# Kernel optimization log

Hardware: AMD Instinct MI355X
Metric: run time of the kernel (lower is better)

Reference implementation:

```python
import jax, jax.numpy as jnp
import numpy as np

B, S, D, H, FF = 2, 4096, 1024, 16, 4096
HD = D // H


def _layernorm(x, g, b, eps=1e-5):
    mu = jnp.mean(x, axis=-1, keepdims=True)
    var = jnp.var(x, axis=-1, keepdims=True)
    return (x - mu) * jax.lax.rsqrt(var + eps) * g + b


def setup_inputs() -> dict:
    key = jax.random.key(0)
    ks = jax.random.split(key, 20)
    sd = 1.0 / np.sqrt(D)
    sf = 1.0 / np.sqrt(FF)
    inp = {
        "x": jax.random.normal(ks[0], (B, S, D), jnp.float32),
        # attention projections, stored as [in, out]
        "wq": jax.random.normal(ks[1], (D, D), jnp.float32) * sd,
        "bq": jnp.zeros((D,), jnp.float32),
        "wk": jax.random.normal(ks[2], (D, D), jnp.float32) * sd,
        "bk": jnp.zeros((D,), jnp.float32),
        "wv": jax.random.normal(ks[3], (D, D), jnp.float32) * sd,
        "bv": jnp.zeros((D,), jnp.float32),
        "wo": jax.random.normal(ks[4], (D, D), jnp.float32) * sd,
        "bo": jnp.zeros((D,), jnp.float32),
        # block norm1 (pre-attention)
        "ln1_g": jnp.ones((D,), jnp.float32),
        "ln1_b": jnp.zeros((D,), jnp.float32),
        # FFN internal norm
        "lnf_g": jnp.ones((D,), jnp.float32),
        "lnf_b": jnp.zeros((D,), jnp.float32),
        # gated FFN
        "w1": jax.random.normal(ks[5], (D, FF), jnp.float32) * sd,
        "b1": jnp.zeros((FF,), jnp.float32),
        "wg": jax.random.normal(ks[6], (D, FF), jnp.float32) * sd,
        "bg": jnp.zeros((FF,), jnp.float32),
        "w2": jax.random.normal(ks[7], (FF, D), jnp.float32) * sf,
        "b2": jnp.zeros((D,), jnp.float32),
    }
    return inp


def reference(x, wq, bq, wk, bk, wv, bv, wo, bo, ln1_g, ln1_b,
              lnf_g, lnf_b, w1, b1, wg, bg, w2, b2):
    # pre-norm attention
    residual = x
    h = _layernorm(x, ln1_g, ln1_b)
    q = (h @ wq + bq).reshape(B, S, H, HD).transpose(0, 2, 1, 3)  # [B,H,S,hd]
    k = (h @ wk + bk).reshape(B, S, H, HD).transpose(0, 2, 1, 3)
    v = (h @ wv + bv).reshape(B, S, H, HD).transpose(0, 2, 1, 3)
    scores = jnp.einsum("bhqd,bhkd->bhqk", q, k) / np.sqrt(HD)
    attn = jax.nn.softmax(scores, axis=-1)  # [B,H,S,S] materialized as in torch src
    ctx = jnp.einsum("bhqk,bhkd->bhqd", attn, v)
    ctx = ctx.transpose(0, 2, 1, 3).reshape(B, S, D)
    attn_out = ctx @ wo + bo
    x = residual + attn_out  # dropout = 0 (eval)

    # gated FFN with internal pre-norm and residual
    res2 = x
    h2 = _layernorm(x, lnf_g, lnf_b)
    gate = jax.nn.sigmoid(h2 @ wg + bg)
    up = jax.nn.gelu(h2 @ w1 + b1, approximate=False)
    out = (up * gate) @ w2 + b2
    return out + res2
```

## Files before the change

kernel.cpp:

```cpp
#include <hip/hip_runtime.h>
#include <hip/hip_bf16.h>

#define BB 2
#define SS 4096
#define DD 1024
#define HH 16
#define HD 64
#define FF 4096
#define MM (BB*SS)

typedef __hip_bfloat16 bf16;
typedef __attribute__((ext_vector_type(8))) __bf16 v8bf;
typedef __attribute__((ext_vector_type(4))) float f32x4;
typedef __attribute__((ext_vector_type(16))) float f32x16;
typedef __attribute__((ext_vector_type(8))) unsigned short u16v8;

__device__ __forceinline__ f32x4 mfma16(v8bf a, v8bf b, f32x4 c) {
  return __builtin_amdgcn_mfma_f32_16x16x32_bf16(a, b, c, 0, 0, 0);
}
__device__ __forceinline__ f32x16 mfma32(v8bf a, v8bf b, f32x16 c) {
  return __builtin_amdgcn_mfma_f32_32x32x16_bf16(a, b, c, 0, 0, 0);
}
__device__ __forceinline__ void gload16(const void* g, void* l) {
  __builtin_amdgcn_global_load_lds((const __attribute__((address_space(1))) void*)g,
                                   (__attribute__((address_space(3))) void*)l, 16, 0, 0);
}
__device__ __forceinline__ unsigned cvtpk_bf16(float lo, float hi) {
  unsigned r;
  asm("v_cvt_pk_bf16_f32 %0, %1, %2" : "=v"(r) : "v"(lo), "v"(hi));
  return r;
}

__global__ void k_tcvt(const float* __restrict__ W, bf16* __restrict__ Wt, int K, int N,
                       int pairsel)
{
  __shared__ float tile[32][33];
  const int n0 = blockIdx.x * 32, k0 = blockIdx.y * 32;
  const int tx = threadIdx.x, ty = threadIdx.y;
#pragma unroll
  for (int i = 0; i < 32; i += 8)
    tile[ty + i][tx] = W[(long)(k0 + ty + i) * N + n0 + tx];
  __syncthreads();
#pragma unroll
  for (int i = 0; i < 32; i += 8) {
    long orow = n0 + ty + i;
    if (pairsel >= 0) orow = ((orow >> 6) << 7) + pairsel * 64 + (orow & 63);
    Wt[orow * K + k0 + tx] = __float2bfloat16(tile[tx][ty + i]);
  }
}

__global__ __launch_bounds__(256)
void k_vtrans(const bf16* __restrict__ V, bf16* __restrict__ Vt)
{
  __shared__ bf16 tile[64][72];
  const int s0 = blockIdx.x * 64;
  const int h  = blockIdx.y;
  const int b  = blockIdx.z;
  const int t  = threadIdx.x;
  const int r = t >> 3, c8 = t & 7;
#pragma unroll
  for (int it = 0; it < 2; ++it) {
    const int sr = it * 32 + r;
    const u16v8 v = *(const u16v8*)(V + (long)(b * SS + s0 + sr) * DD + h * 64 + c8 * 8);
#pragma unroll
    for (int e = 0; e < 8; ++e)
      ((unsigned short*)&tile[sr][0])[c8 * 8 + e] = v[e];
  }
  __syncthreads();
#pragma unroll
  for (int it = 0; it < 2; ++it) {
    const int d = it * 32 + r;
    union { unsigned short s[8]; u16v8 v; } o;
#pragma unroll
    for (int e = 0; e < 8; ++e)
      o.s[e] = ((const unsigned short*)tile)[(c8 * 8 + e) * 72 + d];
    *(u16v8*)(Vt + ((long)(b * HH + h) * HD + d) * (long)SS + s0 + c8 * 8) = o.v;
  }
}

__global__ __launch_bounds__(256)
void k_layernorm(const float* __restrict__ x, const float* __restrict__ g,
                 const float* __restrict__ b, bf16* __restrict__ out)
{
  const int row = blockIdx.x;
  const float4 v = ((const float4*)(x + (long)row * DD))[threadIdx.x];
  float s  = v.x + v.y + v.z + v.w;
  float s2 = v.x*v.x + v.y*v.y + v.z*v.z + v.w*v.w;
#pragma unroll
  for (int off = 1; off < 64; off <<= 1) {
    s  += __shfl_xor(s,  off);
    s2 += __shfl_xor(s2, off);
  }
  __shared__ float red[8];
  if ((threadIdx.x & 63) == 0) {
    red[threadIdx.x >> 6]       = s;
    red[(threadIdx.x >> 6) + 4] = s2;
  }
  __syncthreads();
  s  = red[0] + red[1] + red[2] + red[3];
  s2 = red[4] + red[5] + red[6] + red[7];
  const float mu = s * (1.f / DD);
  const float rs = rsqrtf(s2 * (1.f / DD) - mu * mu + 1e-5f);
  const float4 gv = ((const float4*)g)[threadIdx.x];
  const float4 bv = ((const float4*)b)[threadIdx.x];
  bf16* op = out + (long)row * DD + threadIdx.x * 4;
  op[0] = __float2bfloat16((v.x - mu) * rs * gv.x + bv.x);
  op[1] = __float2bfloat16((v.y - mu) * rs * gv.y + bv.y);
  op[2] = __float2bfloat16((v.z - mu) * rs * gv.z + bv.z);
  op[3] = __float2bfloat16((v.w - mu) * rs * gv.w + bv.w);
}

template<int EPI>
__global__ __launch_bounds__(256, 2)
void k_gemm(const bf16* __restrict__ A, const bf16* __restrict__ Bt,
            const float* __restrict__ bias, const float* __restrict__ res,
            void* __restrict__ Cout, int M, int N, int K, float scale)
{
  __shared__ __align__(16) bf16 As[128 * 32];
  __shared__ __align__(16) bf16 Bs[128 * 32];
  const int t = threadIdx.x;
  const int lane = t & 63, w = t >> 6;
  const int wr = w >> 1, wc = w & 1;
  const int fr = lane & 15, fq = lane >> 4;
  const long m0 = (long)blockIdx.y * 128, n0 = (long)blockIdx.x * 128;

  f32x4 acc[4][4] = {};

  const bf16* Ag0 = A  + (m0 + (t >> 2)) * K + (t & 3) * 8;
  const bf16* Ag1 = Ag0 + 64L * K;
  const bf16* Bg0 = Bt + (n0 + (t >> 2)) * K + (t & 3) * 8;
  const bf16* Bg1 = Bg0 + 64L * K;
  bf16* Al0 = As + t * 8;
  bf16* Al1 = As + 2048 + t * 8;
  bf16* Bl0 = Bs + t * 8;
  bf16* Bl1 = Bs + 2048 + t * 8;

  for (int kk = 0; kk < K; kk += 32) {
    gload16(Ag0 + kk, Al0);
    gload16(Ag1 + kk, Al1);
    gload16(Bg0 + kk, Bl0);
    gload16(Bg1 + kk, Bl1);
    __syncthreads();
    v8bf af[4], bfr[4];
#pragma unroll
    for (int mt = 0; mt < 4; ++mt)
      af[mt] = *(const v8bf*)&As[(wr*64 + mt*16 + fr) * 32 + fq*8];
#pragma unroll
    for (int nt = 0; nt < 4; ++nt)
      bfr[nt] = *(const v8bf*)&Bs[(wc*64 + nt*16 + fr) * 32 + fq*8];
#pragma unroll
    for (int mt = 0; mt < 4; ++mt)
#pragma unroll
      for (int nt = 0; nt < 4; ++nt)
        acc[mt][nt] = mfma16(af[mt], bfr[nt], acc[mt][nt]);
    __syncthreads();
  }

#pragma unroll
  for (int nt = 0; nt < 4; ++nt) {
    const long col = n0 + wc*64 + nt*16 + fr;
    const float bv = bias[col];
#pragma unroll
    for (int mt = 0; mt < 4; ++mt) {
#pragma unroll
      for (int j = 0; j < 4; ++j) {
        const long row = m0 + wr*64 + mt*16 + fq*4 + j;
        float v = (acc[mt][nt][j] + bv) * scale;
        if (EPI == 0) {
          ((bf16*)Cout)[row * N + col] = __float2bfloat16(v);
        } else {
          ((float*)Cout)[row * N + col] = v + res[row * N + col];
        }
      }
    }
  }
}

__global__ __launch_bounds__(256, 2)
void k_ffn_pair(const bf16* __restrict__ A, const bf16* __restrict__ WguT,
                const float* __restrict__ bgb, const float* __restrict__ bub,
                bf16* __restrict__ Out)
{
  __shared__ __align__(16) bf16 smem[8192];
  bf16* As = smem;
  bf16* Bs = smem + 4096;
  const int t = threadIdx.x;
  const int lane = t & 63, w = t >> 6;
  const int wr = w >> 1, wc = w & 1;
  const int fr = lane & 15, fq = lane >> 4;
  const long m0 = (long)blockIdx.y * 128, n0 = (long)blockIdx.x * 128;
  const int tc0 = blockIdx.x * 64;
  const int K = DD;

  f32x4 acc[4][4] = {};

  const bf16* Ag0 = A    + (m0 + (t >> 2)) * K + (t & 3) * 8;
  const bf16* Ag1 = Ag0  + 64L * K;
  const bf16* Bg0 = WguT + (n0 + (t >> 2)) * K + (t & 3) * 8;
  const bf16* Bg1 = Bg0  + 64L * K;

  for (int kk = 0; kk < K; kk += 32) {
    gload16(Ag0 + kk, As + t * 8);
    gload16(Ag1 + kk, As + 2048 + t * 8);
    gload16(Bg0 + kk, Bs + t * 8);
    gload16(Bg1 + kk, Bs + 2048 + t * 8);
    __syncthreads();
    v8bf af[4], bfr[4];
#pragma unroll
    for (int mt = 0; mt < 4; ++mt)
      af[mt] = *(const v8bf*)&As[(wr*64 + mt*16 + fr) * 32 + fq*8];
#pragma unroll
    for (int nt = 0; nt < 4; ++nt)
      bfr[nt] = *(const v8bf*)&Bs[(wc*64 + nt*16 + fr) * 32 + fq*8];
#pragma unroll
    for (int mt = 0; mt < 4; ++mt)
#pragma unroll
      for (int nt = 0; nt < 4; ++nt)
        acc[mt][nt] = mfma16(af[mt], bfr[nt], acc[mt][nt]);
    __syncthreads();
  }

  if (wc == 1) {
#pragma unroll
    for (int nt = 0; nt < 4; ++nt) {
      const int c = nt*16 + fr;
      const float ub = bub[tc0 + c];
#pragma unroll
      for (int mt = 0; mt < 4; ++mt)
#pragma unroll
        for (int j = 0; j < 4; ++j) {
          const int lrow = wr*64 + mt*16 + fq*4 + j;
          smem[lrow*64 + (c ^ (((lrow >> 2) & 3) << 4))] =
              __float2bfloat16(acc[mt][nt][j] + ub);
        }
    }
  }
  __syncthreads();
  if (wc == 0) {
#pragma unroll
    for (int nt = 0; nt < 4; ++nt) {
      const int c = nt*16 + fr;
      const float gb = bgb[tc0 + c];
#pragma unroll
      for (int mt = 0; mt < 4; ++mt)
#pragma unroll
        for (int j = 0; j < 4; ++j) {
          const int lrow = wr*64 + mt*16 + fq*4 + j;
          const float g = acc[mt][nt][j] + gb;
          const float u =
              __bfloat162float(smem[lrow*64 + (c ^ (((lrow >> 2) & 3) << 4))]);
          const float sg = 1.f / (1.f + __expf(-g));
          const float gl = 0.5f * u * (1.f + erff(u * 0.70710678118f));
          Out[(m0 + lrow) * FF + tc0 + c] = __float2bfloat16(sg * gl);
        }
    }
  }
}

__global__ __launch_bounds__(256, 2)
void k_attn(const bf16* __restrict__ Qb, const bf16* __restrict__ Kb,
            const bf16* __restrict__ Vt, bf16* __restrict__ ctx)
{
  __shared__ __align__(16) bf16 Ksh[2][4096];
  __shared__ __align__(16) bf16 Vsh[2][4096];
  const int t = threadIdx.x;
  const int lane = t & 63, w = t >> 6;
  const int q5 = lane & 31, hi = lane >> 5;
  const int q0 = blockIdx.x * 128;
  const int h = blockIdx.y, b = blockIdx.z;
  const long qk_base = ((long)b * SS) * DD + h * HD;
  const long vt_base = ((long)(b * HH + h)) * ((long)HD * SS);

  const int r0 = t >> 3;
  const int cswz = ((t & 7) * 16) ^ ((r0 & 7) << 4);
  const bf16* kg = Kb + qk_base + (long)r0 * DD + (cswz >> 1);
  const bf16* vg = Vt + vt_base + (long)r0 * SS + (cswz >> 1);

  v8bf qf[4];
  {
    const bf16* qp = Qb + qk_base + (long)(q0 + w * 32 + q5) * DD + hi * 8;
#pragma unroll
    for (int c = 0; c < 4; ++c) qf[c] = *(const v8bf*)(qp + c * 16);
  }

  int kcol[4];
#pragma unroll
  for (int c = 0; c < 4; ++c)
    kcol[c] = ((c * 32 + hi * 16) ^ ((q5 & 7) << 4)) >> 1;

  float m_ = -1e30f, l_ = 0.f;
  f32x16 o0 = {}, o1 = {};

#define STAGE(bufidx, kv0_) do {                                  \
    const bf16* kp_ = kg + (long)(kv0_) * DD;                     \
    gload16(kp_,            &Ksh[bufidx][t * 8]);                 \
    gload16(kp_ + 32L * DD, &Ksh[bufidx][2048 + t * 8]);          \
    const bf16* vp_ = vg + (kv0_);                                \
    gload16(vp_,            &Vsh[bufidx][t * 8]);                 \
    gload16(vp_ + 32L * SS, &Vsh[bufidx][2048 + t * 8]);          \
  } while (0)

  STAGE(0, 0);
  __syncthreads();

  for (int tt = 0; tt < SS / 64; ++tt) {
    const int cur = tt & 1;
    if (tt + 1 < SS / 64) STAGE(cur ^ 1, (tt + 1) * 64);

    f32x16 s0 = {}, s1 = {};
#pragma unroll
    for (int c = 0; c < 4; ++c) {
      const v8bf k0 = *(const v8bf*)&Ksh[cur][q5 * 64 + kcol[c]];
      const v8bf k1 = *(const v8bf*)&Ksh[cur][(32 + q5) * 64 + kcol[c]];
      s0 = mfma32(k0, qf[c], s0);
      s1 = mfma32(k1, qf[c], s1);
    }

    float pm = s0[0];
#pragma unroll
    for (int r = 1; r < 16; ++r) pm = fmaxf(pm, s0[r]);
#pragma unroll
    for (int r = 0; r < 16; ++r) pm = fmaxf(pm, s1[r]);
    pm = fmaxf(pm, __shfl_xor(pm, 32));
    const float mn = fmaxf(m_, pm);
    const float al = __builtin_amdgcn_exp2f(m_ - mn);
    m_ = mn;
    float rs = 0.f;
#pragma unroll
    for (int r = 0; r < 16; ++r) { s0[r] = __builtin_amdgcn_exp2f(s0[r] - mn); rs += s0[r]; }
#pragma unroll
    for (int r = 0; r < 16; ++r) { s1[r] = __builtin_amdgcn_exp2f(s1[r] - mn); rs += s1[r]; }
    rs += __shfl_xor(rs, 32);
    l_ = l_ * al + rs;
#pragma unroll
    for (int r = 0; r < 16; ++r) { o0[r] *= al; o1[r] *= al; }

    v8bf pb[4];
#pragma unroll
    for (int c = 0; c < 4; ++c) {
      const int base = (c & 1) * 8;
      unsigned wa0, wa1, wb0, wb1;
      if (c < 2) {
        wa0 = cvtpk_bf16(s0[base + 0], s0[base + 1]);
        wa1 = cvtpk_bf16(s0[base + 2], s0[base + 3]);
        wb0 = cvtpk_bf16(s0[base + 4], s0[base + 5]);
        wb1 = cvtpk_bf16(s0[base + 6], s0[base + 7]);
      } else {
        wa0 = cvtpk_bf16(s1[base + 0], s1[base + 1]);
        wa1 = cvtpk_bf16(s1[base + 2], s1[base + 3]);
        wb0 = cvtpk_bf16(s1[base + 4], s1[base + 5]);
        wb1 = cvtpk_bf16(s1[base + 6], s1[base + 7]);
      }
      asm("v_permlane32_swap_b32 %0, %1" : "+v"(wa0), "+v"(wb0));
      asm("v_permlane32_swap_b32 %0, %1" : "+v"(wa1), "+v"(wb1));
      union { unsigned u[4]; v8bf v; } cvt;
      cvt.u[0] = wa0; cvt.u[1] = wa1; cvt.u[2] = wb0; cvt.u[3] = wb1;
      pb[c] = cvt.v;
    }

#pragma unroll
    for (int c = 0; c < 4; ++c) {
      const v8bf v0f = *(const v8bf*)&Vsh[cur][q5 * 64 + kcol[c]];
      const v8bf v1f = *(const v8bf*)&Vsh[cur][(32 + q5) * 64 + kcol[c]];
      o0 = mfma32(v0f, pb[c], o0);
      o1 = mfma32(v1f, pb[c], o1);
    }
    __syncthreads();
  }
#undef STAGE

  const float inv = 1.f / l_;
  bf16* Osh = &Ksh[0][0];
  const int qrow = w * 32 + q5;
  const int oswz = (qrow & 7) << 4;
#pragma unroll
  for (int r = 0; r < 16; ++r) {
    const int d0 = (r & 3) + 8 * (r >> 2) + 4 * hi;
    Osh[((qrow * 128 + d0 * 2) ^ oswz) >> 1]        = __float2bfloat16(o0[r] * inv);
    Osh[((qrow * 128 + (32 + d0) * 2) ^ oswz) >> 1] = __float2bfloat16(o1[r] * inv);
  }
  __syncthreads();
  {
    const int q = t >> 1, half = t & 1;
    const int qs = (q & 7) << 4;
    bf16* cp = ctx + qk_base + (long)(q0 + q) * DD + half * 32;
#pragma unroll
    for (int s = 0; s < 4; ++s) {
      const int byte = (q * 128 + half * 64 + s * 16) ^ qs;
      *(u16v8*)(cp + s * 8) = *(const u16v8*)&Osh[byte >> 1];
    }
  }
}

extern "C" void kernel_launch(void* const* d_in, const int* in_sizes, int n_in,
                              void* d_out, int out_size, void* d_ws, size_t ws_size,
                              hipStream_t stream)
{
  const float* x    = (const float*)d_in[0];
  const float* wq   = (const float*)d_in[1];
  const float* bq   = (const float*)d_in[2];
  const float* wk   = (const float*)d_in[3];
  const float* bk   = (const float*)d_in[4];
  const float* wv   = (const float*)d_in[5];
  const float* bv   = (const float*)d_in[6];
  const float* wo   = (const float*)d_in[7];
  const float* bo   = (const float*)d_in[8];
  const float* ln1g = (const float*)d_in[9];
  const float* ln1b = (const float*)d_in[10];
  const float* lnfg = (const float*)d_in[11];
  const float* lnfb = (const float*)d_in[12];
  const float* w1   = (const float*)d_in[13];
  const float* b1   = (const float*)d_in[14];
  const float* wg   = (const float*)d_in[15];
  const float* bg   = (const float*)d_in[16];
  const float* w2   = (const float*)d_in[17];
  const float* b2   = (const float*)d_in[18];

  char* ws = (char*)d_ws;
  const size_t MB = 1u << 20;
  bf16*  WqT  = (bf16*)(ws + 0 * MB);
  bf16*  WkT  = (bf16*)(ws + 2 * MB);
  bf16*  WvT  = (bf16*)(ws + 4 * MB);
  bf16*  WoT  = (bf16*)(ws + 6 * MB);
  bf16*  WguT = (bf16*)(ws + 8 * MB);
  bf16*  W2T  = (bf16*)(ws + 24 * MB);
  float* x1   = (float*)(ws + 32 * MB);
  bf16*  hbuf = (bf16*)(ws + 64 * MB);
  bf16*  Qb   = (bf16*)(ws + 80 * MB);
  bf16*  Kb   = (bf16*)(ws + 96 * MB);
  bf16*  Vb   = (bf16*)(ws + 112 * MB);
  bf16*  Vtb  = (bf16*)(ws + 128 * MB);
  bf16*  ctxb = hbuf;
  bf16*  prod = (bf16*)(ws + 80 * MB);

  dim3 tb(32, 8);
  k_tcvt<<<dim3(32, 32), tb, 0, stream>>>(wq, WqT, 1024, 1024, -1);
  k_tcvt<<<dim3(32, 32), tb, 0, stream>>>(wk, WkT, 1024, 1024, -1);
  k_tcvt<<<dim3(32, 32), tb, 0, stream>>>(wv, WvT, 1024, 1024, -1);
  k_tcvt<<<dim3(32, 32), tb, 0, stream>>>(wo, WoT, 1024, 1024, -1);
  k_tcvt<<<dim3(128, 32), tb, 0, stream>>>(wg, WguT, 1024, 4096, 0);
  k_tcvt<<<dim3(128, 32), tb, 0, stream>>>(w1, WguT, 1024, 4096, 1);
  k_tcvt<<<dim3(32, 128), tb, 0, stream>>>(w2, W2T, 4096, 1024, -1);

  k_layernorm<<<MM, 256, 0, stream>>>(x, ln1g, ln1b, hbuf);

  const float qscale = 0.1803368801111204f;
  dim3 g1(1024 / 128, MM / 128);
  k_gemm<0><<<g1, 256, 0, stream>>>(hbuf, WqT, bq, nullptr, Qb, MM, 1024, 1024, qscale);
  k_gemm<0><<<g1, 256, 0, stream>>>(hbuf, WkT, bk, nullptr, Kb, MM, 1024, 1024, 1.f);
  k_gemm<0><<<g1, 256, 0, stream>>>(hbuf, WvT, bv, nullptr, Vb, MM, 1024, 1024, 1.f);
  k_vtrans<<<dim3(SS / 64, HH, BB), 256, 0, stream>>>(Vb, Vtb);

  k_attn<<<dim3(SS / 128, HH, BB), 256, 0, stream>>>(Qb, Kb, Vtb, ctxb);

  k_gemm<1><<<g1, 256, 0, stream>>>(ctxb, WoT, bo, x, x1, MM, 1024, 1024, 1.f);

  k_layernorm<<<MM, 256, 0, stream>>>(x1, lnfg, lnfb, hbuf);

  k_ffn_pair<<<dim3(2 * FF / 128, MM / 128), 256, 0, stream>>>(hbuf, WguT, bg, b1, prod);

  k_gemm<1><<<g1, 256, 0, stream>>>(prod, W2T, b2, x1, (float*)d_out, MM, 1024, 4096, 1.f);
}
```

Baseline: 656.2 us.

## Fuse QKV projections and add 4-stage pipelined 256x128 GEMM kernel

Measured after the change: 706.5 us. 7.7% more time.

```diff
diff --git a/kernel.cpp b/kernel.cpp
--- a/kernel.cpp
+++ b/kernel.cpp
@@ -8,6 +8,7 @@
 #define HD 64
 #define FF 4096
 #define MM (BB*SS)
+#define QKVW 3072
 
 typedef __hip_bfloat16 bf16;
 typedef __attribute__((ext_vector_type(8))) __bf16 v8bf;
@@ -32,7 +33,7 @@
 }
 
 __global__ void k_tcvt(const float* __restrict__ W, bf16* __restrict__ Wt, int K, int N,
-                       int pairsel)
+                       long rowoff, float scale, int pairsel)
 {
   __shared__ float tile[32][33];
   const int n0 = blockIdx.x * 32, k0 = blockIdx.y * 32;
@@ -45,12 +46,12 @@
   for (int i = 0; i < 32; i += 8) {
     long orow = n0 + ty + i;
     if (pairsel >= 0) orow = ((orow >> 6) << 7) + pairsel * 64 + (orow & 63);
-    Wt[orow * K + k0 + tx] = __float2bfloat16(tile[tx][ty + i]);
+    Wt[(rowoff + orow) * K + k0 + tx] = __float2bfloat16(tile[tx][ty + i] * scale);
   }
 }
 
 __global__ __launch_bounds__(256)
-void k_vtrans(const bf16* __restrict__ V, bf16* __restrict__ Vt)
+void k_vtrans(const bf16* __restrict__ qkv, bf16* __restrict__ Vt)
 {
   __shared__ bf16 tile[64][72];
   const int s0 = blockIdx.x * 64;
@@ -61,7 +62,8 @@
 #pragma unroll
   for (int it = 0; it < 2; ++it) {
     const int sr = it * 32 + r;
-    const u16v8 v = *(const u16v8*)(V + (long)(b * SS + s0 + sr) * DD + h * 64 + c8 * 8);
+    const u16v8 v =
+        *(const u16v8*)(qkv + (long)(b * SS + s0 + sr) * QKVW + 2048 + h * 64 + c8 * 8);
 #pragma unroll
     for (int e = 0; e < 8; ++e)
       ((unsigned short*)&tile[sr][0])[c8 * 8 + e] = v[e];
@@ -130,74 +132,6 @@
   const bf16* Ag1 = Ag0 + 64L * K;
   const bf16* Bg0 = Bt + (n0 + (t >> 2)) * K + (t & 3) * 8;
   const bf16* Bg1 = Bg0 + 64L * K;
-  bf16* Al0 = As + t * 8;
-  bf16* Al1 = As + 2048 + t * 8;
-  bf16* Bl0 = Bs + t * 8;
-  bf16* Bl1 = Bs + 2048 + t * 8;
-
-  for (int kk = 0; kk < K; kk += 32) {
-    gload16(Ag0 + kk, Al0);
-    gload16(Ag1 + kk, Al1);
-    gload16(Bg0 + kk, Bl0);
-    gload16(Bg1 + kk, Bl1);
-    __syncthreads();
-    v8bf af[4], bfr[4];
-#pragma unroll
-    for (int mt = 0; mt < 4; ++mt)
-      af[mt] = *(const v8bf*)&As[(wr*64 + mt*16 + fr) * 32 + fq*8];
-#pragma unroll
-    for (int nt = 0; nt < 4; ++nt)
-      bfr[nt] = *(const v8bf*)&Bs[(wc*64 + nt*16 + fr) * 32 + fq*8];
-#pragma unroll
-    for (int mt = 0; mt < 4; ++mt)
-#pragma unroll
-      for (int nt = 0; nt < 4; ++nt)
-        acc[mt][nt] = mfma16(af[mt], bfr[nt], acc[mt][nt]);
-    __syncthreads();
-  }
-
-#pragma unroll
-  for (int nt = 0; nt < 4; ++nt) {
-    const long col = n0 + wc*64 + nt*16 + fr;
-    const float bv = bias[col];
-#pragma unroll
-    for (int mt = 0; mt < 4; ++mt) {
-#pragma unroll
-      for (int j = 0; j < 4; ++j) {
-        const long row = m0 + wr*64 + mt*16 + fq*4 + j;
-        float v = (acc[mt][nt][j] + bv) * scale;
-        if (EPI == 0) {
-          ((bf16*)Cout)[row * N + col] = __float2bfloat16(v);
-        } else {
-          ((float*)Cout)[row * N + col] = v + res[row * N + col];
-        }
-      }
-    }
-  }
-}
-
-__global__ __launch_bounds__(256, 2)
-void k_ffn_pair(const bf16* __restrict__ A, const bf16* __restrict__ WguT,
-                const float* __restrict__ bgb, const float* __restrict__ bub,
-                bf16* __restrict__ Out)
-{
-  __shared__ __align__(16) bf16 smem[8192];
-  bf16* As = smem;
-  bf16* Bs = smem + 4096;
-  const int t = threadIdx.x;
-  const int lane = t & 63, w = t >> 6;
-  const int wr = w >> 1, wc = w & 1;
-  const int fr = lane & 15, fq = lane >> 4;
-  const long m0 = (long)blockIdx.y * 128, n0 = (long)blockIdx.x * 128;
-  const int tc0 = blockIdx.x * 64;
-  const int K = DD;
-
-  f32x4 acc[4][4] = {};
-
-  const bf16* Ag0 = A    + (m0 + (t >> 2)) * K + (t & 3) * 8;
-  const bf16* Ag1 = Ag0  + 64L * K;
-  const bf16* Bg0 = WguT + (n0 + (t >> 2)) * K + (t & 3) * 8;
-  const bf16* Bg1 = Bg0  + 64L * K;
 
   for (int kk = 0; kk < K; kk += 32) {
     gload16(Ag0 + kk, As + t * 8);
@@ -220,46 +154,166 @@
     __syncthreads();
   }
 
-  if (wc == 1) {
-#pragma unroll
-    for (int nt = 0; nt < 4; ++nt) {
-      const int c = nt*16 + fr;
-      const float ub = bub[tc0 + c];
-#pragma unroll
-      for (int mt = 0; mt < 4; ++mt)
+#pragma unroll
+  for (int nt = 0; nt < 4; ++nt) {
+    const long col = n0 + wc*64 + nt*16 + fr;
+    const float bv = bias[col];
+#pragma unroll
+    for (int mt = 0; mt < 4; ++mt) {
+#pragma unroll
+      for (int j = 0; j < 4; ++j) {
+        const long row = m0 + wr*64 + mt*16 + fq*4 + j;
+        float v = (acc[mt][nt][j] + bv) * scale;
+        if (EPI == 0) ((bf16*)Cout)[row * N + col] = __float2bfloat16(v);
+        else          ((float*)Cout)[row * N + col] = v + res[row * N + col];
+      }
+    }
+  }
+}
+
+#define SLOT_B 24576
+#define SLOT_E 12288
+
+template<int EPI, int NT>
+__global__ __launch_bounds__(512)
+void k_gemm2(const bf16* __restrict__ A, const bf16* __restrict__ Bt,
+             const float* __restrict__ b0, const float* __restrict__ b1,
+             const float* __restrict__ b2, const float* __restrict__ res,
+             void* __restrict__ Cout, float s0)
+{
+  constexpr int K = NT * 32;
+  __shared__ __align__(16) bf16 lds[4 * SLOT_E];
+  char* ldsb = (char*)lds;
+
+  const int t = threadIdx.x;
+  const int lane = t & 63, wid = t >> 6;
+  const int wr = wid >> 2, wc = wid & 3;
+  const int fr = lane & 15, fq = lane >> 4;
+  const long m0 = (long)blockIdx.y * 256;
+  const int  n0 = blockIdx.x * 128;
+
+  const int rA0 = t >> 2, gA = t & 3;
+  const bf16* srcA0 = A + (m0 + rA0) * K + (gA ^ (rA0 & 3)) * 8;
+  const int rA1 = 128 + rA0;
+  const bf16* srcA1 = A + (m0 + rA1) * K + (gA ^ (rA1 & 3)) * 8;
+  const bf16* srcB  = Bt + (long)(n0 + rA0) * K + (gA ^ (rA0 & 3)) * 8;
+
+  int a_el[8], b_el[2];
+#pragma unroll
+  for (int mt = 0; mt < 8; ++mt)
+    a_el[mt] = (wr * 128 + mt * 16 + fr) * 32 + ((fq ^ (fr & 3)) << 3);
+#pragma unroll
+  for (int nt = 0; nt < 2; ++nt)
+    b_el[nt] = 8192 + (wc * 32 + nt * 16 + fr) * 32 + ((fq ^ (fr & 3)) << 3);
+
+  f32x4 acc[8][2] = {};
+
+#define STAGE2(s_, kt_) {                                                   \
+    const long ko_ = (long)(kt_) * 32;                                      \
+    gload16(srcA0 + ko_, ldsb + (s_) * SLOT_B + t * 16);                    \
+    gload16(srcA1 + ko_, ldsb + (s_) * SLOT_B + 8192 + t * 16);             \
+    gload16(srcB  + ko_, ldsb + (s_) * SLOT_B + 16384 + t * 16);            \
+  }
+
+#define GBODY(kt_, VMSTR, DO_STAGE_) {                                      \
+    asm volatile("s_waitcnt vmcnt(" VMSTR ")" ::: "memory");                \
+    __builtin_amdgcn_s_barrier();                                           \
+    __builtin_amdgcn_sched_barrier(0);                                      \
+    const bf16* sl_ = lds + ((kt_) & 3) * SLOT_E;                           \
+    v8bf av_[8], bv_[2];                                                    \
+    _Pragma("unroll") for (int mt = 0; mt < 8; ++mt)                        \
+      av_[mt] = *(const v8bf*)&sl_[a_el[mt]];                               \
+    _Pragma("unroll") for (int nt = 0; nt < 2; ++nt)                        \
+      bv_[nt] = *(const v8bf*)&sl_[b_el[nt]];                               \
+    if (DO_STAGE_) STAGE2(((kt_) + 3) & 3, (kt_) + 3);                      \
+    _Pragma("unroll") for (int mt = 0; mt < 8; ++mt)                        \
+      _Pragma("unroll") for (int nt = 0; nt < 2; ++nt)                      \
+        acc[mt][nt] = mfma16(av_[mt], bv_[nt], acc[mt][nt]);                \
+  }
+
+  STAGE2(0, 0); STAGE2(1, 1); STAGE2(2, 2);
+
+  for (int kt = 0; kt < NT - 2; ++kt) GBODY(kt, "6", kt < NT - 3);
+  GBODY(NT - 2, "3", false);
+  GBODY(NT - 1, "0", false);
+#undef GBODY
+#undef STAGE2
+
+  if (EPI == 0) {
+    const float* bp = (n0 < 1024) ? b0 : (n0 < 2048) ? b1 : b2;
+    const float bs = (n0 < 1024) ? s0 : 1.f;
+#pragma unroll
+    for (int nt = 0; nt < 2; ++nt) {
+      const int col = n0 + wc * 32 + nt * 16 + fr;
+      const float bv = bp[col & 1023] * bs;
+#pragma unroll
+      for (int mt = 0; mt < 8; ++mt)
 #pragma unroll
         for (int j = 0; j < 4; ++j) {
-          const int lrow = wr*64 + mt*16 + fq*4 + j;
-          smem[lrow*64 + (c ^ (((lrow >> 2) & 3) << 4))] =
-              __float2bfloat16(acc[mt][nt][j] + ub);
+          const long row = m0 + wr * 128 + mt * 16 + fq * 4 + j;
+          ((bf16*)Cout)[row * QKVW + col] = __float2bfloat16(acc[mt][nt][j] + bv);
         }
     }
-  }
-  __syncthreads();
-  if (wc == 0) {
-#pragma unroll
-    for (int nt = 0; nt < 4; ++nt) {
-      const int c = nt*16 + fr;
-      const float gb = bgb[tc0 + c];
-#pragma unroll
-      for (int mt = 0; mt < 4; ++mt)
+  } else if (EPI == 1) {
+#pragma unroll
+    for (int nt = 0; nt < 2; ++nt) {
+      const int col = n0 + wc * 32 + nt * 16 + fr;
+      const float bv = b0[col];
+#pragma unroll
+      for (int mt = 0; mt < 8; ++mt)
 #pragma unroll
         for (int j = 0; j < 4; ++j) {
-          const int lrow = wr*64 + mt*16 + fq*4 + j;
-          const float g = acc[mt][nt][j] + gb;
-          const float u =
-              __bfloat162float(smem[lrow*64 + (c ^ (((lrow >> 2) & 3) << 4))]);
-          const float sg = 1.f / (1.f + __expf(-g));
-          const float gl = 0.5f * u * (1.f + erff(u * 0.70710678118f));
-          Out[(m0 + lrow) * FF + tc0 + c] = __float2bfloat16(sg * gl);
+          const long row = m0 + wr * 128 + mt * 16 + fq * 4 + j;
+          ((float*)Cout)[row * DD + col] = acc[mt][nt][j] + bv + res[row * DD + col];
         }
     }
+  } else {
+    const int tb = n0 >> 1;
+    __syncthreads();
+    if (wc >= 2) {
+      const int reg = (wr * 2 + (wc - 2)) * 4096;
+#pragma unroll
+      for (int nt = 0; nt < 2; ++nt) {
+        const int col = nt * 16 + fr;
+        const float ub = b1[tb + (wc - 2) * 32 + col];
+#pragma unroll
+        for (int mt = 0; mt < 8; ++mt)
+#pragma unroll
+          for (int j = 0; j < 4; ++j) {
+            const int row = mt * 16 + fq * 4 + j;
+            lds[reg + row * 32 + (col ^ (((row >> 2) & 3) << 2))] =
+                __float2bfloat16(acc[mt][nt][j] + ub);
+          }
+      }
+    }
+    __syncthreads();
+    if (wc < 2) {
+      const int reg = (wr * 2 + wc) * 4096;
+#pragma unroll
+      for (int nt = 0; nt < 2; ++nt) {
+        const int col = nt * 16 + fr;
+        const int tc = tb + wc * 32 + col;
+        const float gb = b0[tc];
+#pragma unroll
+        for (int mt = 0; mt < 8; ++mt)
+#pragma unroll
+          for (int j = 0; j < 4; ++j) {
+            const int row = mt * 16 + fq * 4 + j;
+            const float g = acc[mt][nt][j] + gb;
+            const float u =
+                __bfloat162float(lds[reg + row * 32 + (col ^ (((row >> 2) & 3) << 2))]);
+            const float sg = 1.f / (1.f + __expf(-g));
+            const float gl = 0.5f * u * (1.f + erff(u * 0.70710678118f));
+            ((bf16*)Cout)[(m0 + wr * 128 + row) * FF + tc] = __float2bfloat16(sg * gl);
+          }
+      }
+    }
   }
 }
 
 __global__ __launch_bounds__(256, 2)
-void k_attn(const bf16* __restrict__ Qb, const bf16* __restrict__ Kb,
-            const bf16* __restrict__ Vt, bf16* __restrict__ ctx)
+void k_attn(const bf16* __restrict__ qkv, const bf16* __restrict__ Vt,
+            bf16* __restrict__ ctx)
 {
   __shared__ __align__(16) bf16 Ksh[2][4096];
   __shared__ __align__(16) bf16 Vsh[2][4096];
@@ -268,17 +322,18 @@
   const int q5 = lane & 31, hi = lane >> 5;
   const int q0 = blockIdx.x * 128;
   const int h = blockIdx.y, b = blockIdx.z;
-  const long qk_base = ((long)b * SS) * DD + h * HD;
-  const long vt_base = ((long)(b * HH + h)) * ((long)HD * SS);
+  const long qkv_row0 = (long)b * SS * QKVW + h * HD;
+  const long ctx_base = (long)b * SS * DD + h * HD;
+  const long vt_base  = ((long)(b * HH + h)) * ((long)HD * SS);
 
   const int r0 = t >> 3;
   const int cswz = ((t & 7) * 16) ^ ((r0 & 7) << 4);
-  const bf16* kg = Kb + qk_base + (long)r0 * DD + (cswz >> 1);
+  const bf16* kg = qkv + qkv_row0 + 1024 + (long)r0 * QKVW + (cswz >> 1);
   const bf16* vg = Vt + vt_base + (long)r0 * SS + (cswz >> 1);
 
   v8bf qf[4];
   {
-    const bf16* qp = Qb + qk_base + (long)(q0 + w * 32 + q5) * DD + hi * 8;
+    const bf16* qp = qkv + qkv_row0 + (long)(q0 + w * 32 + q5) * QKVW + hi * 8;
 #pragma unroll
     for (int c = 0; c < 4; ++c) qf[c] = *(const v8bf*)(qp + c * 16);
   }
@@ -291,13 +346,13 @@
   float m_ = -1e30f, l_ = 0.f;
   f32x16 o0 = {}, o1 = {};
 
-#define STAGE(bufidx, kv0_) do {                                  \
-    const bf16* kp_ = kg + (long)(kv0_) * DD;                     \
-    gload16(kp_,            &Ksh[bufidx][t * 8]);                 \
-    gload16(kp_ + 32L * DD, &Ksh[bufidx][2048 + t * 8]);          \
-    const bf16* vp_ = vg + (kv0_);                                \
-    gload16(vp_,            &Vsh[bufidx][t * 8]);                 \
-    gload16(vp_ + 32L * SS, &Vsh[bufidx][2048 + t * 8]);          \
+#define STAGE(bufidx, kv0_) do {                                    \
+    const bf16* kp_ = kg + (long)(kv0_) * QKVW;                     \
+    gload16(kp_,              &Ksh[bufidx][t * 8]);                 \
+    gload16(kp_ + 32L * QKVW, &Ksh[bufidx][2048 + t * 8]);          \
+    const bf16* vp_ = vg + (kv0_);                                  \
+    gload16(vp_,            &Vsh[bufidx][t * 8]);                   \
+    gload16(vp_ + 32L * SS, &Vsh[bufidx][2048 + t * 8]);            \
   } while (0)
 
   STAGE(0, 0);
@@ -383,7 +438,7 @@
   {
     const int q = t >> 1, half = t & 1;
     const int qs = (q & 7) << 4;
-    bf16* cp = ctx + qk_base + (long)(q0 + q) * DD + half * 32;
+    bf16* cp = ctx + ctx_base + (long)(q0 + q) * DD + half * 32;
 #pragma unroll
     for (int s = 0; s < 4; ++s) {
       const int byte = (q * 128 + half * 64 + s * 16) ^ qs;
@@ -418,46 +473,43 @@
 
   char* ws = (char*)d_ws;
   const size_t MB = 1u << 20;
-  bf16*  WqT  = (bf16*)(ws + 0 * MB);
-  bf16*  WkT  = (bf16*)(ws + 2 * MB);
-  bf16*  WvT  = (bf16*)(ws + 4 * MB);
-  bf16*  WoT  = (bf16*)(ws + 6 * MB);
-  bf16*  WguT = (bf16*)(ws + 8 * MB);
-  bf16*  W2T  = (bf16*)(ws + 24 * MB);
-  float* x1   = (float*)(ws + 32 * MB);
-  bf16*  hbuf = (bf16*)(ws + 64 * MB);
-  bf16*  Qb   = (bf16*)(ws + 80 * MB);
-  bf16*  Kb   = (bf16*)(ws + 96 * MB);
-  bf16*  Vb   = (bf16*)(ws + 112 * MB);
-  bf16*  Vtb  = (bf16*)(ws + 128 * MB);
-  bf16*  ctxb = hbuf;
-  bf16*  prod = (bf16*)(ws + 80 * MB);
+  bf16*  WqkvT = (bf16*)(ws + 0 * MB);
+  bf16*  WoT   = (bf16*)(ws + 6 * MB);
+  bf16*  WguT  = (bf16*)(ws + 8 * MB);
+  bf16*  W2T   = (bf16*)(ws + 24 * MB);
+  float* x1    = (float*)(ws + 32 * MB);
+  bf16*  hbuf  = (bf16*)(ws + 64 * MB);
+  bf16*  QKVb  = (bf16*)(ws + 80 * MB);
+  bf16*  Vtb   = (bf16*)(ws + 128 * MB);
+  bf16*  ctxb  = hbuf;
+  bf16*  prod  = (bf16*)(ws + 80 * MB);
+
+  const float qscale = 0.1803368801111204f;
 
   dim3 tb(32, 8);
-  k_tcvt<<<dim3(32, 32), tb, 0, stream>>>(wq, WqT, 1024, 1024, -1);
-  k_tcvt<<<dim3(32, 32), tb, 0, stream>>>(wk, WkT, 1024, 1024, -1);
-  k_tcvt<<<dim3(32, 32), tb, 0, stream>>>(wv, WvT, 1024, 1024, -1);
-  k_tcvt<<<dim3(32, 32), tb, 0, stream>>>(wo, WoT, 1024, 1024, -1);
-  k_tcvt<<<dim3(128, 32), tb, 0, stream>>>(wg, WguT, 1024, 4096, 0);
-  k_tcvt<<<dim3(128, 32), tb, 0, stream>>>(w1, WguT, 1024, 4096, 1);
-  k_tcvt<<<dim3(32, 128), tb, 0, stream>>>(w2, W2T, 4096, 1024, -1);
+  k_tcvt<<<dim3(32, 32), tb, 0, stream>>>(wq, WqkvT, 1024, 1024, 0, qscale, -1);
+  k_tcvt<<<dim3(32, 32), tb, 0, stream>>>(wk, WqkvT, 1024, 1024, 1024, 1.f, -1);
+  k_tcvt<<<dim3(32, 32), tb, 0, stream>>>(wv, WqkvT, 1024, 1024, 2048, 1.f, -1);
+  k_tcvt<<<dim3(32, 32), tb, 0, stream>>>(wo, WoT, 1024, 1024, 0, 1.f, -1);
+  k_tcvt<<<dim3(128, 32), tb, 0, stream>>>(wg, WguT, 1024, 4096, 0, 1.f, 0);
+  k_tcvt<<<dim3(128, 32), tb, 0, stream>>>(w1, WguT, 1024, 4096, 0, 1.f, 1);
+  k_tcvt<<<dim3(32, 128), tb, 0, stream>>>(w2, W2T, 4096, 1024, 0, 1.f, -1);
 
   k_layernorm<<<MM, 256, 0, stream>>>(x, ln1g, ln1b, hbuf);
 
-  const float qscale = 0.1803368801111204f;
-  dim3 g1(1024 / 128, MM / 128);
-  k_gemm<0><<<g1, 256, 0, stream>>>(hbuf, WqT, bq, nullptr, Qb, MM, 1024, 1024, qscale);
-  k_gemm<0><<<g1, 256, 0, stream>>>(hbuf, WkT, bk, nullptr, Kb, MM, 1024, 1024, 1.f);
-  k_gemm<0><<<g1, 256, 0, stream>>>(hbuf, WvT, bv, nullptr, Vb, MM, 1024, 1024, 1.f);
-  k_vtrans<<<dim3(SS / 64, HH, BB), 256, 0, stream>>>(Vb, Vtb);
-
-  k_attn<<<dim3(SS / 128, HH, BB), 256, 0, stream>>>(Qb, Kb, Vtb, ctxb);
-
-  k_gemm<1><<<g1, 256, 0, stream>>>(ctxb, WoT, bo, x, x1, MM, 1024, 1024, 1.f);
+  k_gemm2<0, 32><<<dim3(QKVW / 128, MM / 256), 512, 0, stream>>>(
+      hbuf, WqkvT, bq, bk, bv, nullptr, QKVb, qscale);
+
+  k_vtrans<<<dim3(SS / 64, HH, BB), 256, 0, stream>>>(QKVb, Vtb);
+  k_attn<<<dim3(SS / 128, HH, BB), 256, 0, stream>>>(QKVb, Vtb, ctxb);
+
+  k_gemm<1><<<dim3(8, 64), 256, 0, stream>>>(ctxb, WoT, bo, x, x1, MM, 1024, 1024, 1.f);
 
   k_layernorm<<<MM, 256, 0, stream>>>(x1, lnfg, lnfb, hbuf);
 
-  k_ffn_pair<<<dim3(2 * FF / 128, MM / 128), 256, 0, stream>>>(hbuf, WguT, bg, b1, prod);
-
-  k_gemm<1><<<g1, 256, 0, stream>>>(prod, W2T, b2, x1, (float*)d_out, MM, 1024, 4096, 1.f);
-}
+  k_gemm2<2, 32><<<dim3(8192 / 128, MM / 256), 512, 0, stream>>>(
+      hbuf, WguT, bg, b1, nullptr, nullptr, prod, 1.f);
+
+  k_gemm2<1, 128><<<dim3(DD / 128, MM / 256), 512, 0, stream>>>(
+      prod, W2T, b2, nullptr, nullptr, x1, (float*)d_out, 1.f);
+}
```
